# Kernel optimization log

Hardware: AMD Instinct MI355X
Metric: run time of the kernel (lower is better)

Reference implementation:

```python
import jax, jax.numpy as jnp
import numpy as np

BF = 0.3  # blend_fraction


def setup_inputs() -> dict:
    B, T, V, D = 32, 8192, 2820, 64
    rng = np.random.default_rng(0)
    bmask = rng.random((B, T)) < 0.15
    bmask[:, 0] = False
    seg = np.cumsum(bmask, axis=1)                      # segment index per frame
    seg_ids = rng.integers(1, V, size=(B, T))           # one id per segment (avoid padding idx 0)
    ids = np.take_along_axis(seg_ids, seg, axis=1).astype(np.int64)
    key = jax.random.key(0)
    table = jax.random.normal(key, (V, D), dtype=jnp.float32)
    return {"ids": jnp.asarray(ids), "table": table}


def _blend_weights(ids):
    """Vectorized duration-proportional boundary blending.
    Returns (blend_weights (B,T) f32, neighbor_ids (B,T) int)."""
    B, T = ids.shape
    pos = jnp.arange(T)[None, :]                        # (1,T)
    boundary = ids[:, :-1] != ids[:, 1:]                # (B,T-1)
    is_start = jnp.concatenate([jnp.ones((B, 1), bool), boundary], axis=1)
    is_end = jnp.concatenate([boundary, jnp.ones((B, 1), bool)], axis=1)
    # per-position segment [start, end)
    start = jax.lax.cummax(jnp.where(is_start, pos, 0), axis=1)
    end = jax.lax.cummin(jnp.where(is_end, pos + 1, T), axis=1, reverse=True)
    dur = end - start                                    # current segment duration
    dur_prev = jnp.take_along_axis(dur, jnp.clip(start - 1, 0), axis=1)
    dur_next = jnp.take_along_axis(dur, jnp.minimum(end, T - 1), axis=1)
    prev_id = jnp.take_along_axis(ids, jnp.clip(start - 1, 0), axis=1)
    next_id = jnp.take_along_axis(ids, jnp.minimum(end, T - 1), axis=1)

    f32 = jnp.float32
    # --- boundary at end-1 (left-side ramp toward next phoneme) ---
    rad_n = (BF * jnp.minimum(dur, dur_next)).astype(f32)
    valid_n = (end < T) & (rad_n >= 0.5)
    rn = jnp.maximum(1, jnp.round(rad_n).astype(jnp.int32))  # round half-to-even, matches Python round
    left_start = jnp.maximum(0, end - rn)
    w_n = jnp.minimum(0.5 * (pos - left_start + 1).astype(f32) / rn.astype(f32), 0.5)
    w_n = jnp.where(valid_n & (pos >= left_start), w_n, 0.0)

    # --- boundary at start-1 (right-side ramp toward previous phoneme) ---
    rad_p = (BF * jnp.minimum(dur_prev, dur)).astype(f32)
    valid_p = (start > 0) & (rad_p >= 0.5)
    rp = jnp.maximum(1, jnp.round(rad_p).astype(jnp.int32))
    right_end = jnp.minimum(T, start + rp)
    w_p = jnp.minimum(0.5 * (right_end - pos).astype(f32) / rp.astype(f32), 0.5)
    w_p = jnp.where(valid_p & (pos < right_end), w_p, 0.0)

    # boundaries are processed left-to-right; a later (next) boundary only
    # overwrites with strictly greater weight -> ties keep the prev-boundary id
    w = jnp.maximum(w_p, w_n)
    neighbor = jnp.where(w_n > w_p, next_id, jnp.where(w_p > 0.0, prev_id, ids))
    return w, neighbor


def reference(ids, table):
    tbl = table.at[0].set(0.0)          # padding_idx=0
    w, neighbor = _blend_weights(ids)
    emb = tbl[ids]                      # (B,T,D)
    nemb = tbl[neighbor]                # (B,T,D)
    w3 = w[..., None]
    return (1.0 - w3) * emb + w3 * nemb
```

## Files before the change

### kernel.cpp

```cpp
#include <hip/hip_runtime.h>


#define BFC   0.3f
#define TILE  256
#define HALO  768
#define SSTAGE (TILE + 2 * HALO)
#define NWORD  (SSTAGE / 64)
#define NTH    256

__device__ __forceinline__ int seg_start_global(const int* __restrict__ row, int t) {
    while (t > 0 && row[t] == row[t - 1]) --t;
    return t;
}
__device__ __forceinline__ int seg_end_global(const int* __restrict__ row, int t, int T) {
    ++t;
    while (t < T && row[t] == row[t - 1]) ++t;
    return t;
}

__device__ __forceinline__ int bits_le(const unsigned long long* bm, int li) {
    int wi = li >> 6, bi = li & 63;
    unsigned long long m = bm[wi] & (~0ULL >> (63 - bi));
    while (m == 0ULL && wi > 0) m = bm[--wi];
    return m ? ((wi << 6) + 63 - __clzll((long long)m)) : -1;
}
__device__ __forceinline__ int bits_gt(const unsigned long long* bm, int li) {
    int wi = li >> 6, bi = li & 63;
    unsigned long long m = (bi == 63) ? 0ULL : (bm[wi] & (~0ULL << (bi + 1)));
    while (m == 0ULL && wi < NWORD - 1) m = bm[++wi];
    return m ? ((wi << 6) + (__ffsll((unsigned long long)m) - 1)) : -1;
}

__global__ __launch_bounds__(NTH) void blur_phoneme_kernel(
    const int* __restrict__ ids, const float* __restrict__ table,
    float* __restrict__ out, int T, int D)
{
    __shared__ int sid[SSTAGE];
    __shared__ unsigned long long bmask[NWORD];
    __shared__ float s_w[TILE];
    __shared__ int s_nb[TILE];

    const int b   = blockIdx.y;
    const int t0  = blockIdx.x * TILE;
    const int tid = threadIdx.x;
    const int* __restrict__ row = ids + (size_t)b * T;

    for (int i = tid; i < SSTAGE; i += NTH) {
        int t = t0 - HALO + i;
        sid[i] = (t >= 0 && t < T) ? row[t] : 0;
    }
    __syncthreads();

    for (int i = tid; i < SSTAGE; i += NTH) {
        int t = t0 - HALO + i;
        bool pred;
        if (t <= 0)      pred = (t == 0);
        else if (t >= T) pred = true;
        else {
            int prv = (i >= 1) ? sid[i - 1] : row[t - 1];
            pred = (sid[i] != prv);
        }
        unsigned long long m = __ballot(pred);
        if ((tid & 63) == 0) bmask[i >> 6] = m;
    }
    __syncthreads();

    {
        const int li = HALO + tid;
        const int t  = t0 + tid;
        int s_loc = bits_le(bmask, li);
        int e_loc = bits_gt(bmask, li);
        int start = (s_loc >= 0) ? (t0 - HALO + s_loc) : seg_start_global(row, t);
        int end   = (e_loc >= 0) ? (t0 - HALO + e_loc) : seg_end_global(row, t, T);
        int dur   = end - start;
        int myid  = sid[li];

        float w_n = 0.f, w_p = 0.f;
        int nid = myid, pid = myid;

        if (end < T) {
            int nxt_id, nend;
            if (e_loc >= 0) {
                nxt_id = sid[e_loc];
                int n_loc = bits_gt(bmask, e_loc);
                nend = (n_loc >= 0) ? (t0 - HALO + n_loc) : seg_end_global(row, end, T);
            } else {
                nxt_id = row[end];
                nend = seg_end_global(row, end, T);
            }
            float rad_n = BFC * (float)min(dur, nend - end);
            if (rad_n >= 0.5f) {
                int rn = max(1, (int)rintf(rad_n));
                int left_start = max(0, end - rn);
                if (t >= left_start) {
                    w_n = fminf(0.5f * (float)(t - left_start + 1) / (float)rn, 0.5f);
                    nid = nxt_id;
                }
            }
        }
        if (start > 0) {
            int prv_id, pstart;
            if (s_loc >= 1) {
                prv_id = sid[s_loc - 1];
                int p_loc = bits_le(bmask, s_loc - 1);
                pstart = (p_loc >= 0) ? (t0 - HALO + p_loc) : seg_start_global(row, start - 1);
            } else {
                prv_id = row[start - 1];
                pstart = seg_start_global(row, start - 1);
            }
            float rad_p = BFC * (float)min(start - pstart, dur);
            if (rad_p >= 0.5f) {
                int rp = max(1, (int)rintf(rad_p));
                int right_end = min(T, start + rp);
                if (t < right_end) {
                    w_p = fminf(0.5f * (float)(right_end - t) / (float)rp, 0.5f);
                    pid = prv_id;
                }
            }
        }
        s_w[tid]  = fmaxf(w_p, w_n);
        s_nb[tid] = (w_n > w_p) ? nid : ((w_p > 0.f) ? pid : myid);
    }
    __syncthreads();

    const int DC = D >> 2;
    const float4* __restrict__ tbl4 = reinterpret_cast<const float4*>(table);
    float4* __restrict__ out4 = reinterpret_cast<float4*>(out);
    size_t base = ((size_t)b * T + t0) * DC;
    for (int idx = tid; idx < TILE * DC; idx += NTH) {
        int p = idx / DC;
        int c = idx - p * DC;
        int id = sid[HALO + p];
        int nb = s_nb[p];
        float w = s_w[p];
        float4 ea = (id != 0) ? tbl4[(size_t)id * DC + c] : float4{0.f, 0.f, 0.f, 0.f};
        float4 eb = (nb == id) ? ea
                  : ((nb != 0) ? tbl4[(size_t)nb * DC + c] : float4{0.f, 0.f, 0.f, 0.f});
        float a = 1.0f - w;
        float4 o;
        o.x = a * ea.x + w * eb.x;
        o.y = a * ea.y + w * eb.y;
        o.z = a * ea.z + w * eb.z;
        o.w = a * ea.w + w * eb.w;
        out4[base + idx] = o;
    }
}

extern "C" void kernel_launch(void* const* d_in, const int* in_sizes, int n_in,
                              void* d_out, int out_size, void* d_ws, size_t ws_size,
                              hipStream_t stream) {
    const int*   ids   = (const int*)d_in[0];
    const float* table = (const float*)d_in[1];
    float*       out   = (float*)d_out;

    const int n_ids = in_sizes[0];
    const int D = out_size / n_ids;
    const int T = 8192;
    const int B = n_ids / T;

    dim3 grid(T / TILE, B);
    blur_phoneme_kernel<<<grid, NTH, 0, stream>>>(ids, table, out, T, D);
}
```

Before: 87.20 us.

## Shrink halo, hardcode sizes, pack weights, unroll gathers with nontemporal stores

Shrinks the staged halo from 768 to 256 ids, so less id data is loaded and scanned per block. T and D become compile-time constants so the loops can be fully unrolled. Weight and neighbour id are packed into one float2 in shared memory, and the zero-id branches become multiplicative masks that always load both table rows. Output is written with nontemporal stores. The smaller halo relies more often on the slow global segment-walk fallback when a segment crosses the halo, and fixed D=64/T=8192 limits generality.

```diff
diff --git a/kernel.cpp b/kernel.cpp
--- a/kernel.cpp
+++ b/kernel.cpp
@@ -1,20 +1,24 @@
 #include <hip/hip_runtime.h>
 
 
-#define BFC   0.3f
-#define TILE  256
-#define HALO  768
+#define BFC    0.3f
+#define TLEN   8192
+#define TILE   256
+#define HALO   256
 #define SSTAGE (TILE + 2 * HALO)
 #define NWORD  (SSTAGE / 64)
 #define NTH    256
+#define DC     16
+
+typedef float f4 __attribute__((ext_vector_type(4)));
 
 __device__ __forceinline__ int seg_start_global(const int* __restrict__ row, int t) {
     while (t > 0 && row[t] == row[t - 1]) --t;
     return t;
 }
-__device__ __forceinline__ int seg_end_global(const int* __restrict__ row, int t, int T) {
+__device__ __forceinline__ int seg_end_global(const int* __restrict__ row, int t) {
     ++t;
-    while (t < T && row[t] == row[t - 1]) ++t;
+    while (t < TLEN && row[t] == row[t - 1]) ++t;
     return t;
 }
 
@@ -28,34 +32,37 @@
     int wi = li >> 6, bi = li & 63;
     unsigned long long m = (bi == 63) ? 0ULL : (bm[wi] & (~0ULL << (bi + 1)));
     while (m == 0ULL && wi < NWORD - 1) m = bm[++wi];
-    return m ? ((wi << 6) + (__ffsll((unsigned long long)m) - 1)) : -1;
+    return m ? ((wi << 6) + (__ffsll(m) - 1)) : -1;
 }
 
 __global__ __launch_bounds__(NTH) void blur_phoneme_kernel(
     const int* __restrict__ ids, const float* __restrict__ table,
-    float* __restrict__ out, int T, int D)
+    float* __restrict__ out)
 {
     __shared__ int sid[SSTAGE];
     __shared__ unsigned long long bmask[NWORD];
-    __shared__ float s_w[TILE];
-    __shared__ int s_nb[TILE];
+    __shared__ float2 s_wn[TILE];
 
     const int b   = blockIdx.y;
     const int t0  = blockIdx.x * TILE;
     const int tid = threadIdx.x;
-    const int* __restrict__ row = ids + (size_t)b * T;
+    const int* __restrict__ row = ids + (size_t)b * TLEN;
 
-    for (int i = tid; i < SSTAGE; i += NTH) {
+    #pragma unroll
+    for (int k = 0; k < SSTAGE / NTH; ++k) {
+        int i = tid + k * NTH;
         int t = t0 - HALO + i;
-        sid[i] = (t >= 0 && t < T) ? row[t] : 0;
+        sid[i] = (t >= 0 && t < TLEN) ? row[t] : 0;
     }
     __syncthreads();
 
-    for (int i = tid; i < SSTAGE; i += NTH) {
+    #pragma unroll
+    for (int k = 0; k < SSTAGE / NTH; ++k) {
+        int i = tid + k * NTH;
         int t = t0 - HALO + i;
         bool pred;
-        if (t <= 0)      pred = (t == 0);
-        else if (t >= T) pred = true;
+        if (t <= 0)         pred = (t == 0);
+        else if (t >= TLEN) pred = true;
         else {
             int prv = (i >= 1) ? sid[i - 1] : row[t - 1];
             pred = (sid[i] != prv);
@@ -71,22 +78,22 @@
         int s_loc = bits_le(bmask, li);
         int e_loc = bits_gt(bmask, li);
         int start = (s_loc >= 0) ? (t0 - HALO + s_loc) : seg_start_global(row, t);
-        int end   = (e_loc >= 0) ? (t0 - HALO + e_loc) : seg_end_global(row, t, T);
+        int end   = (e_loc >= 0) ? (t0 - HALO + e_loc) : seg_end_global(row, t);
         int dur   = end - start;
         int myid  = sid[li];
 
         float w_n = 0.f, w_p = 0.f;
         int nid = myid, pid = myid;
 
-        if (end < T) {
+        if (end < TLEN) {
             int nxt_id, nend;
             if (e_loc >= 0) {
                 nxt_id = sid[e_loc];
                 int n_loc = bits_gt(bmask, e_loc);
-                nend = (n_loc >= 0) ? (t0 - HALO + n_loc) : seg_end_global(row, end, T);
+                nend = (n_loc >= 0) ? (t0 - HALO + n_loc) : seg_end_global(row, end);
             } else {
                 nxt_id = row[end];
-                nend = seg_end_global(row, end, T);
+                nend = seg_end_global(row, end);
             }
             float rad_n = BFC * (float)min(dur, nend - end);
             if (rad_n >= 0.5f) {
@@ -111,38 +118,36 @@
             float rad_p = BFC * (float)min(start - pstart, dur);
             if (rad_p >= 0.5f) {
                 int rp = max(1, (int)rintf(rad_p));
-                int right_end = min(T, start + rp);
+                int right_end = min(TLEN, start + rp);
                 if (t < right_end) {
                     w_p = fminf(0.5f * (float)(right_end - t) / (float)rp, 0.5f);
                     pid = prv_id;
                 }
             }
         }
-        s_w[tid]  = fmaxf(w_p, w_n);
-        s_nb[tid] = (w_n > w_p) ? nid : ((w_p > 0.f) ? pid : myid);
+        float w = fmaxf(w_p, w_n);
+        int nb = (w_n > w_p) ? nid : ((w_p > 0.f) ? pid : myid);
+        s_wn[tid] = make_float2(w, __int_as_float(nb));
     }
     __syncthreads();
 
-    const int DC = D >> 2;
-    const float4* __restrict__ tbl4 = reinterpret_cast<const float4*>(table);
-    float4* __restrict__ out4 = reinterpret_cast<float4*>(out);
-    size_t base = ((size_t)b * T + t0) * DC;
-    for (int idx = tid; idx < TILE * DC; idx += NTH) {
-        int p = idx / DC;
-        int c = idx - p * DC;
+    const f4* __restrict__ tbl4 = reinterpret_cast<const f4*>(table);
+    f4* __restrict__ out4 = reinterpret_cast<f4*>(out) + ((size_t)b * TLEN + t0) * DC;
+    const int c  = tid & (DC - 1);
+    const int p0 = tid >> 4;
+    #pragma unroll
+    for (int k = 0; k < TILE * DC / NTH; ++k) {
+        int p = p0 + (k << 4);
         int id = sid[HALO + p];
-        int nb = s_nb[p];
-        float w = s_w[p];
-        float4 ea = (id != 0) ? tbl4[(size_t)id * DC + c] : float4{0.f, 0.f, 0.f, 0.f};
-        float4 eb = (nb == id) ? ea
-                  : ((nb != 0) ? tbl4[(size_t)nb * DC + c] : float4{0.f, 0.f, 0.f, 0.f});
-        float a = 1.0f - w;
-        float4 o;
-        o.x = a * ea.x + w * eb.x;
-        o.y = a * ea.y + w * eb.y;
-        o.z = a * ea.z + w * eb.z;
-        o.w = a * ea.w + w * eb.w;
-        out4[base + idx] = o;
+        float2 wn = s_wn[p];
+        int nb = __float_as_int(wn.y);
+        float w = wn.x;
+        f4 ea = tbl4[id * DC + c];
+        f4 eb = tbl4[nb * DC + c];
+        float wa = (id != 0) ? (1.0f - w) : 0.0f;
+        float wb = (nb != 0) ? w : 0.0f;
+        f4 o = ea * wa + eb * wb;
+        __builtin_nontemporal_store(o, &out4[tid + (k << 8)]);
     }
 }
 
@@ -154,10 +159,8 @@
     float*       out   = (float*)d_out;
 
     const int n_ids = in_sizes[0];
-    const int D = out_size / n_ids;
-    const int T = 8192;
-    const int B = n_ids / T;
+    const int B = n_ids / TLEN;
 
-    dim3 grid(T / TILE, B);
-    blur_phoneme_kernel<<<grid, NTH, 0, stream>>>(ids, table, out, T, D);
+    dim3 grid(TLEN / TILE, B);
+    blur_phoneme_kernel<<<grid, NTH, 0, stream>>>(ids, table, out);
 }
```

After: 82.55 us. -5.3%, faster.
